# Optimization experiments

Measured on AMD Instinct MI355X. Metric: run time of the kernel, lower is better.

## Reference

```python
import jax, jax.numpy as jnp
import numpy as np
from jax import lax

CHANNEL = 64
HIDDEN = 128

def _conv(x, w, b):
    # x: [B, Cin, H, W], w: [Cout, Cin, 3, 3] -> [B, Cout, H, W], SAME padding
    y = lax.conv_general_dilated(x, w, window_strides=(1, 1), padding='SAME',
                                 dimension_numbers=('NCHW', 'OIHW', 'NCHW'))
    return y + b[None, :, None, None]

def setup_inputs() -> dict:
    key = jax.random.key(0)
    ks = jax.random.split(key, 5)
    T, B, C, H, W = 12, 2, CHANNEL, 128, 128
    x = jax.random.normal(ks[0], (T, B, C, H, W), dtype=jnp.float32)
    fan_g = (C + HIDDEN) * 9
    W_gates = jax.random.normal(ks[1], (4 * HIDDEN, C + HIDDEN, 3, 3), dtype=jnp.float32) / np.sqrt(fan_g)
    b_gates = jnp.zeros((4 * HIDDEN,), dtype=jnp.float32)
    W_out = jax.random.normal(ks[2], (C, HIDDEN, 3, 3), dtype=jnp.float32) / np.sqrt(HIDDEN * 9)
    b_out = jnp.zeros((C,), dtype=jnp.float32)
    return {'x': x, 'W_gates': W_gates, 'b_gates': b_gates, 'W_out': W_out, 'b_out': b_out}

def _convlstm_forward(x, W_gates, b_gates, W_out, b_out):
    T, B, C, H, W = x.shape
    h0 = jnp.zeros((B, HIDDEN, H, W), dtype=x.dtype)
    c0 = jnp.zeros((B, HIDDEN, H, W), dtype=x.dtype)

    def step(carry, xt):
        h, c = carry
        gates = _conv(jnp.concatenate([xt, h], axis=1), W_gates, b_gates)
        i_g, f_g, o_g, g_g = jnp.split(gates, 4, axis=1)
        c = jax.nn.sigmoid(f_g) * c + jax.nn.sigmoid(i_g) * jnp.tanh(g_g)
        h = jax.nn.sigmoid(o_g) * jnp.tanh(c)
        return (h, c), h

    _, hs = lax.scan(step, (h0, c0), x)          # hs: [T, B, HIDDEN, H, W]
    out = _conv(hs.reshape(T * B, HIDDEN, H, W), W_out, b_out)
    return out.reshape(T, B, C, H, W)

def reference(x, W_gates, b_gates, W_out, b_out):
    return _convlstm_forward(x, W_gates, b_gates, W_out, b_out)
```

## Files before the change

### kernel.cpp

```cpp
#include <hip/hip_runtime.h>

typedef _Float16 f16;
typedef __attribute__((ext_vector_type(8))) _Float16 f16x8;
typedef __attribute__((ext_vector_type(4))) _Float16 f16x4;
typedef __attribute__((ext_vector_type(4))) float f32x4;

#define SLICE_H 4326400


__device__ __forceinline__ void gld_lds16(void* lds, const void* g) {
  __builtin_amdgcn_global_load_lds(
      (const __attribute__((address_space(1))) void*)g,
      (__attribute__((address_space(3))) void*)lds, 16, 0, 0);
}

__device__ __forceinline__ float sigf(float v) { return 1.0f / (1.0f + __expf(-v)); }
__device__ __forceinline__ float tanh_fast(float v) { return 2.0f / (1.0f + __expf(-2.0f * v)) - 1.0f; }


__global__ __launch_bounds__(256) void kwt(const float* __restrict__ wsrc,
                                           f16* __restrict__ th, int R) {
  int idx = blockIdx.x * 256 + threadIdx.x;
  if (idx >= 9 * R) return;
  int tap = idx / R, r = idx - tap * R;
  th[idx] = (f16)wsrc[(size_t)r * 9 + tap];
}


__global__ __launch_bounds__(256) void kxform(const float* __restrict__ xt,
                                              f16* __restrict__ xp) {
  int pid = blockIdx.x * 256 + threadIdx.x;
  int b = pid >> 14, y = (pid >> 7) & 127, x = pid & 127;
  const float* src = xt + (size_t)b * 64 * 16384 + (size_t)y * 128 + x;
  size_t doff = ((size_t)((b * 130 + y + 1) * 130 + (x + 1))) * 64;
#pragma unroll
  for (int cc = 0; cc < 8; ++cc) {
    f16x8 vh;
#pragma unroll
    for (int j = 0; j < 8; ++j) vh[j] = (f16)src[(size_t)(cc * 8 + j) * 16384];
    *(f16x8*)(xp + doff + cc * 8) = vh;
  }
}


#define SMEM_G (25344 + 49152)

__global__ __launch_bounds__(512, 4) void kgates(
    const f16* __restrict__ xp, const f16* __restrict__ hp,
    const f16* __restrict__ wg, f16* __restrict__ gates) {
  extern __shared__ char smem[];
  f16* Ap = (f16*)smem;
  f16* Br = (f16*)(smem + 25344);
  const int tid = threadIdx.x;
  const int lane = tid & 63;
  const int w = tid >> 6;
  const int y = blockIdx.x;
  const int b = blockIdx.y;
  const int n0 = blockIdx.z * 256;
  const int wm = w >> 2, wn = w & 3;
  const int chunk = (lane & 3) ^ ((lane >> 3) & 3);

  f32x4 acc[4][4] = {};

  auto stageA = [&](int cig) {
    const f16* S; int CS, cigl;
    if (cig < 2) { S = xp; CS = 64;  cigl = cig; }
    else         { S = hp; CS = 128; cigl = cig - 2; }
    for (int i = w; i < 27; i += 8) {
      int dy = i / 9, sub = i - dy * 9;
      int xp0 = sub * 16;
      const f16* src = S +
          ((size_t)((b * 130 + y + dy) * 130 + xp0 + (lane >> 2))) * CS +
          cigl * 32 + chunk * 8;
      f16* dst = Ap + (dy * 132 + xp0) * 32;
      if (sub == 8) { if (lane < 16) gld_lds16(dst, src); }
      else gld_lds16(dst, src);
    }
  };
  auto stageB = [&](int j) {
    int cig = j / 9, tap = j - cig * 9;
    f16* dst = Br + (j % 3) * 8192;
    for (int i = w; i < 16; i += 8) {
      const f16* src = wg +
          ((size_t)(tap * 512 + n0 + i * 16 + (lane >> 2))) * 192 +
          cig * 32 + chunk * 8;
      gld_lds16(dst + i * 512, src);
    }
  };

  stageA(0);
  stageB(0);
  stageB(1);
  asm volatile("s_waitcnt vmcnt(2)" ::: "memory");
  __builtin_amdgcn_s_barrier();

  for (int j = 0; j < 54; ++j) {
    const int cig = j / 9, tap = j - cig * 9;
    const int dy = tap / 3, dx = tap - dy * 3;
    const int q = lane >> 4;
    const f16* Bc = Br + (j % 3) * 8192;
    f16x8 af[4], bfr[4];
#pragma unroll
    for (int mf = 0; mf < 4; ++mf) {
      int r = wm * 64 + mf * 16 + (lane & 15) + dx;
      af[mf] = *(const f16x8*)(Ap + (dy * 132 + r) * 32 + ((q ^ ((r >> 1) & 3)) << 3));
    }
#pragma unroll
    for (int nf = 0; nf < 4; ++nf) {
      int n = wn * 64 + nf * 16 + (lane & 15);
      bfr[nf] = *(const f16x8*)(Bc + n * 32 + ((q ^ ((n >> 1) & 3)) << 3));
    }
    if (j + 2 < 54) stageB(j + 2);
    __builtin_amdgcn_s_setprio(1);
#pragma unroll
    for (int mf = 0; mf < 4; ++mf)
#pragma unroll
      for (int nf = 0; nf < 4; ++nf)
        acc[mf][nf] = __builtin_amdgcn_mfma_f32_16x16x32_f16(af[mf], bfr[nf], acc[mf][nf], 0, 0, 0);
    __builtin_amdgcn_s_setprio(0);
    if (tap == 8) {
      __builtin_amdgcn_s_barrier();
      if (cig < 5) stageA(cig + 1);
      asm volatile("s_waitcnt vmcnt(0)" ::: "memory");
      __builtin_amdgcn_s_barrier();
    } else {
      if (j + 2 < 54) asm volatile("s_waitcnt vmcnt(2)" ::: "memory");
      else            asm volatile("s_waitcnt vmcnt(0)" ::: "memory");
      __builtin_amdgcn_s_barrier();
    }
  }

  size_t pixbase = ((size_t)(b * 128 + y)) * 128;
#pragma unroll
  for (int mf = 0; mf < 4; ++mf) {
#pragma unroll
    for (int nf = 0; nf < 4; ++nf) {
      int cout = n0 + wn * 64 + nf * 16 + (lane & 15);
#pragma unroll
      for (int r = 0; r < 4; ++r) {
        int x = wm * 64 + mf * 16 + (lane >> 4) * 4 + r;
        gates[(pixbase + x) * 512 + cout] = (f16)acc[mf][nf][r];
      }
    }
  }
}


__global__ __launch_bounds__(256) void kpoint(const f16* __restrict__ gates,
                                              const float* __restrict__ bg,
                                              float* __restrict__ cbuf,
                                              f16* __restrict__ hslot) {
  int gid = blockIdx.x * 256 + threadIdx.x;
  int pixel = gid >> 5, cq = gid & 31;
  int b = pixel >> 14, y = (pixel >> 7) & 127, x = pixel & 127;
  size_t gb = (size_t)pixel * 512 + cq * 4;
  const f16x4 ig = *(const f16x4*)(gates + gb);
  const f16x4 fg = *(const f16x4*)(gates + gb + 128);
  const f16x4 og = *(const f16x4*)(gates + gb + 256);
  const f16x4 gg = *(const f16x4*)(gates + gb + 384);
  const f32x4 bi  = *(const f32x4*)(bg + cq * 4);
  const f32x4 bff = *(const f32x4*)(bg + cq * 4 + 128);
  const f32x4 boo = *(const f32x4*)(bg + cq * 4 + 256);
  const f32x4 bgg = *(const f32x4*)(bg + cq * 4 + 384);
  f32x4 co = *(const f32x4*)(cbuf + (size_t)pixel * 128 + cq * 4);
  f32x4 cn;
  f16x4 hh;
#pragma unroll
  for (int j = 0; j < 4; ++j) {
    float iv = sigf((float)ig[j] + bi[j]);
    float fv = sigf((float)fg[j] + bff[j]);
    float ov = sigf((float)og[j] + boo[j]);
    float gv = tanh_fast((float)gg[j] + bgg[j]);
    float cv = fv * co[j] + iv * gv;
    float hv = ov * tanh_fast(cv);
    cn[j] = cv;
    hh[j] = (f16)hv;
  }
  *(f32x4*)(cbuf + (size_t)pixel * 128 + cq * 4) = cn;
  size_t hoff = ((size_t)((b * 130 + y + 1) * 130 + (x + 1))) * 128 + cq * 4;
  *(f16x4*)(hslot + hoff) = hh;
}


#define SMEM_O (25344 + 12288)

__global__ __launch_bounds__(256, 4) void koutconv(
    const f16* __restrict__ hr, int slot0, const f16* __restrict__ wo,
    const float* __restrict__ bo, float* __restrict__ outb) {
  extern __shared__ char smem[];
  f16* Ap = (f16*)smem;
  f16* Br = (f16*)(smem + 25344);
  const int tid = threadIdx.x, lane = tid & 63, w = tid >> 6;
  const int y = blockIdx.x;
  const int b = blockIdx.y;
  const int ts = blockIdx.z;
  const f16* hp = hr + (size_t)((slot0 + ts) % 5) * SLICE_H;
  float* outt = outb + (size_t)ts * 2 * 64 * 16384;
  const int chunk = (lane & 3) ^ ((lane >> 3) & 3);

  f32x4 acc[2][4] = {};

  auto stageA = [&](int cig) {
    for (int i = w; i < 27; i += 4) {
      int dy = i / 9, sub = i - dy * 9;
      int xp0 = sub * 16;
      const f16* src = hp +
          ((size_t)((b * 130 + y + dy) * 130 + xp0 + (lane >> 2))) * 128 +
          cig * 32 + chunk * 8;
      f16* dst = Ap + (dy * 132 + xp0) * 32;
      if (sub == 8) { if (lane < 16) gld_lds16(dst, src); }
      else gld_lds16(dst, src);
    }
  };
  auto stageB = [&](int j) {
    int cig = j / 9, tap = j - cig * 9;
    const f16* src = wo +
        ((size_t)(tap * 64 + w * 16 + (lane >> 2))) * 128 +
        cig * 32 + chunk * 8;
    gld_lds16(Br + (j % 3) * 2048 + w * 512, src);
  };

  stageA(0);
  stageB(0);
  stageB(1);
  asm volatile("s_waitcnt vmcnt(1)" ::: "memory");
  __builtin_amdgcn_s_barrier();

  for (int j = 0; j < 36; ++j) {
    const int cig = j / 9, tap = j - cig * 9;
    const int dy = tap / 3, dx = tap - dy * 3;
    const int q = lane >> 4;
    const f16* Bc = Br + (j % 3) * 2048;
    f16x8 af[2], bfr[4];
#pragma unroll
    for (int mf = 0; mf < 2; ++mf) {
      int r = w * 32 + mf * 16 + (lane & 15) + dx;
      af[mf] = *(const f16x8*)(Ap + (dy * 132 + r) * 32 + ((q ^ ((r >> 1) & 3)) << 3));
    }
#pragma unroll
    for (int nf = 0; nf < 4; ++nf) {
      int n = nf * 16 + (lane & 15);
      bfr[nf] = *(const f16x8*)(Bc + n * 32 + ((q ^ ((n >> 1) & 3)) << 3));
    }
    if (j + 2 < 36) stageB(j + 2);
    __builtin_amdgcn_s_setprio(1);
#pragma unroll
    for (int mf = 0; mf < 2; ++mf)
#pragma unroll
      for (int nf = 0; nf < 4; ++nf)
        acc[mf][nf] = __builtin_amdgcn_mfma_f32_16x16x32_f16(af[mf], bfr[nf], acc[mf][nf], 0, 0, 0);
    __builtin_amdgcn_s_setprio(0);
    if (tap == 8) {
      __builtin_amdgcn_s_barrier();
      if (cig < 3) stageA(cig + 1);
      asm volatile("s_waitcnt vmcnt(0)" ::: "memory");
      __builtin_amdgcn_s_barrier();
    } else {
      if (j + 2 < 36) asm volatile("s_waitcnt vmcnt(1)" ::: "memory");
      else            asm volatile("s_waitcnt vmcnt(0)" ::: "memory");
      __builtin_amdgcn_s_barrier();
    }
  }

#pragma unroll
  for (int nf = 0; nf < 4; ++nf) {
    int cout = nf * 16 + (lane & 15);
    float bias = bo[cout];
#pragma unroll
    for (int mf = 0; mf < 2; ++mf) {
      int xbase = w * 32 + mf * 16 + (lane >> 4) * 4;
      f32x4 v = acc[mf][nf];
      v[0] += bias; v[1] += bias; v[2] += bias; v[3] += bias;
      *(f32x4*)(outt + (((size_t)b * 64 + cout) * 128 + y) * 128 + xbase) = v;
    }
  }
}


extern "C" void kernel_launch(void* const* d_in, const int* in_sizes, int n_in,
                              void* d_out, int out_size, void* d_ws, size_t ws_size,
                              hipStream_t stream) {
  const float* x  = (const float*)d_in[0];
  const float* Wg = (const float*)d_in[1];
  const float* bg = (const float*)d_in[2];
  const float* Wo = (const float*)d_in[3];
  const float* bo = (const float*)d_in[4];
  float* out = (float*)d_out;

  char* base = (char*)d_ws;
  size_t off = 0;
  auto carve = [&](size_t bytes) {
    char* p = base + off;
    off += (bytes + 1023) & ~(size_t)1023;
    return p;
  };
  const size_t PADPOS = (size_t)2 * 130 * 130;
  const size_t xpad_b  = PADPOS * 64 * 2 + 1024;
  const size_t hring_b = (size_t)5 * SLICE_H * 2 + 1024;
  const size_t c_b = (size_t)2 * 128 * 128 * 128 * 4;
  const size_t g_b = (size_t)2 * 128 * 128 * 512 * 2;

  f16* xp    = (f16*)carve(xpad_b);
  f16* hr    = (f16*)carve(hring_b);
  float* cbuf = (float*)carve(c_b);
  f16* gates = (f16*)carve(g_b);
  f16* wg    = (f16*)carve((size_t)9 * 512 * 192 * 2);
  f16* wo    = (f16*)carve((size_t)9 * 64 * 128 * 2);

  hipMemsetAsync(xp, 0, xpad_b, stream);
  hipMemsetAsync(hr, 0, hring_b, stream);
  hipMemsetAsync(cbuf, 0, c_b, stream);

  kwt<<<(9 * 512 * 192 + 255) / 256, 256, 0, stream>>>(Wg, wg, 512 * 192);
  kwt<<<(9 * 64 * 128 + 255) / 256, 256, 0, stream>>>(Wo, wo, 64 * 128);

  for (int t = 0; t < 12; ++t) {
    const float* xt = x + (size_t)t * 2 * 64 * 16384;
    kxform<<<128, 256, 0, stream>>>(xt, xp);
    kgates<<<dim3(128, 2, 2), 512, SMEM_G, stream>>>(
        xp, hr + (size_t)(t % 5) * SLICE_H, wg, gates);
    kpoint<<<4096, 256, 0, stream>>>(gates, bg, cbuf,
        hr + (size_t)((t + 1) % 5) * SLICE_H);
    if ((t & 3) == 3) {
      koutconv<<<dim3(128, 2, 4), 256, SMEM_O, stream>>>(
          hr, (t - 2) % 5, wo, bo, out + (size_t)(t - 3) * 2 * 64 * 16384);
    }
  }
}
```

Before: 1.134 ms.

## Fuse LSTM pointwise update into gates conv epilogue via gate-interleaved weights

Reorders the gate weight rows so that each wave's output tile holds the i, f, o and g gates for the same 16 hidden channels. This lets the conv kernel apply the sigmoid/tanh cell update in registers and write c and h directly, removing the fp16 gates buffer round-trip and the separate pointwise launch per timestep. In exchange the block shrinks to 4 waves, each holding an 8x4 accumulator tile, which doubles accumulator registers per thread and halves waves per block. The loops are also restructured so the ring-buffer slot is tracked incrementally instead of computed with a modulo.

```diff
diff --git a/kernel.cpp b/kernel.cpp
--- a/kernel.cpp
+++ b/kernel.cpp
@@ -26,6 +26,18 @@
   th[idx] = (f16)wsrc[(size_t)r * 9 + tap];
 }
 
+__global__ __launch_bounds__(256) void kwtg(const float* __restrict__ wsrc,
+                                            f16* __restrict__ th) {
+  int idx = blockIdx.x * 256 + threadIdx.x;
+  const int R = 512 * 192;
+  if (idx >= 9 * R) return;
+  int tap = idx / R, rr = idx - tap * R;
+  int co = rr / 192, ci = rr - co * 192;
+  int gate = co >> 7, hch = co & 127;
+  int N = ((hch >> 6) << 8) + (((hch & 63) >> 4) << 6) + (gate << 4) + (hch & 15);
+  th[(size_t)tap * R + (size_t)N * 192 + ci] = (f16)wsrc[(size_t)rr * 9 + tap];
+}
+
 
 __global__ __launch_bounds__(256) void kxform(const float* __restrict__ xt,
                                               f16* __restrict__ xp) {
@@ -45,9 +57,10 @@
 
 #define SMEM_G (25344 + 49152)
 
-__global__ __launch_bounds__(512, 4) void kgates(
+__global__ __launch_bounds__(256, 2) void kgates(
     const f16* __restrict__ xp, const f16* __restrict__ hp,
-    const f16* __restrict__ wg, f16* __restrict__ gates) {
+    const f16* __restrict__ wg, const float* __restrict__ bg,
+    float* __restrict__ cbuf, f16* __restrict__ hslot) {
   extern __shared__ char smem[];
   f16* Ap = (f16*)smem;
   f16* Br = (f16*)(smem + 25344);
@@ -56,17 +69,17 @@
   const int w = tid >> 6;
   const int y = blockIdx.x;
   const int b = blockIdx.y;
-  const int n0 = blockIdx.z * 256;
-  const int wm = w >> 2, wn = w & 3;
+  const int z = blockIdx.z;
+  const int n0 = z * 256;
   const int chunk = (lane & 3) ^ ((lane >> 3) & 3);
 
-  f32x4 acc[4][4] = {};
+  f32x4 acc[8][4] = {};
 
   auto stageA = [&](int cig) {
     const f16* S; int CS, cigl;
     if (cig < 2) { S = xp; CS = 64;  cigl = cig; }
     else         { S = hp; CS = 128; cigl = cig - 2; }
-    for (int i = w; i < 27; i += 8) {
+    for (int i = w; i < 27; i += 4) {
       int dy = i / 9, sub = i - dy * 9;
       int xp0 = sub * 16;
       const f16* src = S +
@@ -77,10 +90,9 @@
       else gld_lds16(dst, src);
     }
   };
-  auto stageB = [&](int j) {
-    int cig = j / 9, tap = j - cig * 9;
-    f16* dst = Br + (j % 3) * 8192;
-    for (int i = w; i < 16; i += 8) {
+  auto stageB = [&](int cig, int tap, int slot) {
+    f16* dst = Br + slot * 8192;
+    for (int i = w; i < 16; i += 4) {
       const f16* src = wg +
           ((size_t)(tap * 512 + n0 + i * 16 + (lane >> 2))) * 192 +
           cig * 32 + chunk * 8;
@@ -89,96 +101,78 @@
   };
 
   stageA(0);
-  stageB(0);
-  stageB(1);
-  asm volatile("s_waitcnt vmcnt(2)" ::: "memory");
+  stageB(0, 0, 0);
+  stageB(0, 1, 1);
+  asm volatile("s_waitcnt vmcnt(4)" ::: "memory");
   __builtin_amdgcn_s_barrier();
 
-  for (int j = 0; j < 54; ++j) {
-    const int cig = j / 9, tap = j - cig * 9;
-    const int dy = tap / 3, dx = tap - dy * 3;
-    const int q = lane >> 4;
-    const f16* Bc = Br + (j % 3) * 8192;
-    f16x8 af[4], bfr[4];
-#pragma unroll
-    for (int mf = 0; mf < 4; ++mf) {
-      int r = wm * 64 + mf * 16 + (lane & 15) + dx;
-      af[mf] = *(const f16x8*)(Ap + (dy * 132 + r) * 32 + ((q ^ ((r >> 1) & 3)) << 3));
-    }
-#pragma unroll
-    for (int nf = 0; nf < 4; ++nf) {
-      int n = wn * 64 + nf * 16 + (lane & 15);
-      bfr[nf] = *(const f16x8*)(Bc + n * 32 + ((q ^ ((n >> 1) & 3)) << 3));
-    }
-    if (j + 2 < 54) stageB(j + 2);
-    __builtin_amdgcn_s_setprio(1);
-#pragma unroll
-    for (int mf = 0; mf < 4; ++mf)
-#pragma unroll
-      for (int nf = 0; nf < 4; ++nf)
-        acc[mf][nf] = __builtin_amdgcn_mfma_f32_16x16x32_f16(af[mf], bfr[nf], acc[mf][nf], 0, 0, 0);
-    __builtin_amdgcn_s_setprio(0);
-    if (tap == 8) {
-      __builtin_amdgcn_s_barrier();
-      if (cig < 5) stageA(cig + 1);
-      asm volatile("s_waitcnt vmcnt(0)" ::: "memory");
-      __builtin_amdgcn_s_barrier();
-    } else {
-      if (j + 2 < 54) asm volatile("s_waitcnt vmcnt(2)" ::: "memory");
-      else            asm volatile("s_waitcnt vmcnt(0)" ::: "memory");
-      __builtin_amdgcn_s_barrier();
-    }
-  }
-
-  size_t pixbase = ((size_t)(b * 128 + y)) * 128;
-#pragma unroll
-  for (int mf = 0; mf < 4; ++mf) {
-#pragma unroll
-    for (int nf = 0; nf < 4; ++nf) {
-      int cout = n0 + wn * 64 + nf * 16 + (lane & 15);
-#pragma unroll
-      for (int r = 0; r < 4; ++r) {
-        int x = wm * 64 + mf * 16 + (lane >> 4) * 4 + r;
-        gates[(pixbase + x) * 512 + cout] = (f16)acc[mf][nf][r];
-      }
-    }
-  }
-}
-
-
-__global__ __launch_bounds__(256) void kpoint(const f16* __restrict__ gates,
-                                              const float* __restrict__ bg,
-                                              float* __restrict__ cbuf,
-                                              f16* __restrict__ hslot) {
-  int gid = blockIdx.x * 256 + threadIdx.x;
-  int pixel = gid >> 5, cq = gid & 31;
-  int b = pixel >> 14, y = (pixel >> 7) & 127, x = pixel & 127;
-  size_t gb = (size_t)pixel * 512 + cq * 4;
-  const f16x4 ig = *(const f16x4*)(gates + gb);
-  const f16x4 fg = *(const f16x4*)(gates + gb + 128);
-  const f16x4 og = *(const f16x4*)(gates + gb + 256);
-  const f16x4 gg = *(const f16x4*)(gates + gb + 384);
-  const f32x4 bi  = *(const f32x4*)(bg + cq * 4);
-  const f32x4 bff = *(const f32x4*)(bg + cq * 4 + 128);
-  const f32x4 boo = *(const f32x4*)(bg + cq * 4 + 256);
-  const f32x4 bgg = *(const f32x4*)(bg + cq * 4 + 384);
-  f32x4 co = *(const f32x4*)(cbuf + (size_t)pixel * 128 + cq * 4);
-  f32x4 cn;
-  f16x4 hh;
-#pragma unroll
-  for (int j = 0; j < 4; ++j) {
-    float iv = sigf((float)ig[j] + bi[j]);
-    float fv = sigf((float)fg[j] + bff[j]);
-    float ov = sigf((float)og[j] + boo[j]);
-    float gv = tanh_fast((float)gg[j] + bgg[j]);
-    float cv = fv * co[j] + iv * gv;
-    float hv = ov * tanh_fast(cv);
-    cn[j] = cv;
-    hh[j] = (f16)hv;
-  }
-  *(f32x4*)(cbuf + (size_t)pixel * 128 + cq * 4) = cn;
-  size_t hoff = ((size_t)((b * 130 + y + 1) * 130 + (x + 1))) * 128 + cq * 4;
-  *(f16x4*)(hslot + hoff) = hh;
+  int sl = 0;
+  for (int cig = 0; cig < 6; ++cig) {
+    for (int tap = 0; tap < 9; ++tap) {
+      const int j = cig * 9 + tap;
+      const int dy = tap / 3, dx = tap - dy * 3;
+      const int q = lane >> 4;
+      const f16* Bc = Br + sl * 8192;
+      f16x8 af[8], bfr[4];
+#pragma unroll
+      for (int mf = 0; mf < 8; ++mf) {
+        int r = mf * 16 + (lane & 15) + dx;
+        af[mf] = *(const f16x8*)(Ap + (dy * 132 + r) * 32 + ((q ^ ((r >> 1) & 3)) << 3));
+      }
+#pragma unroll
+      for (int nf = 0; nf < 4; ++nf) {
+        int n = w * 64 + nf * 16 + (lane & 15);
+        bfr[nf] = *(const f16x8*)(Bc + n * 32 + ((q ^ ((n >> 1) & 3)) << 3));
+      }
+      if (j + 2 < 54) {
+        int j2 = j + 2;
+        stageB(j2 / 9, j2 % 9, (sl + 2 >= 3) ? sl - 1 : sl + 2);
+      }
+      __builtin_amdgcn_s_setprio(1);
+#pragma unroll
+      for (int mf = 0; mf < 8; ++mf)
+#pragma unroll
+        for (int nf = 0; nf < 4; ++nf)
+          acc[mf][nf] = __builtin_amdgcn_mfma_f32_16x16x32_f16(af[mf], bfr[nf], acc[mf][nf], 0, 0, 0);
+      __builtin_amdgcn_s_setprio(0);
+      if (tap == 8) {
+        __builtin_amdgcn_s_barrier();
+        if (cig < 5) stageA(cig + 1);
+        asm volatile("s_waitcnt vmcnt(0)" ::: "memory");
+        __builtin_amdgcn_s_barrier();
+      } else {
+        if (j + 2 < 54) asm volatile("s_waitcnt vmcnt(4)" ::: "memory");
+        else            asm volatile("s_waitcnt vmcnt(0)" ::: "memory");
+        __builtin_amdgcn_s_barrier();
+      }
+      sl = (sl + 1 >= 3) ? 0 : sl + 1;
+    }
+  }
+
+  const int lch = w * 16 + (lane & 15);
+  const int hch = z * 64 + lch;
+  const float bi  = bg[hch];
+  const float bf2 = bg[128 + hch];
+  const float bo2 = bg[256 + hch];
+  const float bg2 = bg[384 + hch];
+  const size_t pixbase = ((size_t)(b * 128 + y)) * 128;
+  const size_t hbase = ((size_t)((b * 130 + y + 1) * 130 + 1)) * 128 + hch;
+#pragma unroll
+  for (int mf = 0; mf < 8; ++mf) {
+#pragma unroll
+    for (int r = 0; r < 4; ++r) {
+      int px = mf * 16 + (lane >> 4) * 4 + r;
+      size_t cidx = (pixbase + px) * 128 + hch;
+      float co = cbuf[cidx];
+      float iv = sigf(acc[mf][0][r] + bi);
+      float fv = sigf(acc[mf][1][r] + bf2);
+      float ov = sigf(acc[mf][2][r] + bo2);
+      float gv = tanh_fast(acc[mf][3][r] + bg2);
+      float cv = fv * co + iv * gv;
+      cbuf[cidx] = cv;
+      hslot[hbase + (size_t)px * 128] = (f16)(ov * tanh_fast(cv));
+    }
+  }
 }
 
 
@@ -212,53 +206,57 @@
       else gld_lds16(dst, src);
     }
   };
-  auto stageB = [&](int j) {
+  auto stageB = [&](int j, int slot) {
     int cig = j / 9, tap = j - cig * 9;
     const f16* src = wo +
         ((size_t)(tap * 64 + w * 16 + (lane >> 2))) * 128 +
         cig * 32 + chunk * 8;
-    gld_lds16(Br + (j % 3) * 2048 + w * 512, src);
+    gld_lds16(Br + slot * 2048 + w * 512, src);
   };
 
   stageA(0);
-  stageB(0);
-  stageB(1);
+  stageB(0, 0);
+  stageB(1, 1);
   asm volatile("s_waitcnt vmcnt(1)" ::: "memory");
   __builtin_amdgcn_s_barrier();
 
-  for (int j = 0; j < 36; ++j) {
-    const int cig = j / 9, tap = j - cig * 9;
-    const int dy = tap / 3, dx = tap - dy * 3;
-    const int q = lane >> 4;
-    const f16* Bc = Br + (j % 3) * 2048;
-    f16x8 af[2], bfr[4];
-#pragma unroll
-    for (int mf = 0; mf < 2; ++mf) {
-      int r = w * 32 + mf * 16 + (lane & 15) + dx;
-      af[mf] = *(const f16x8*)(Ap + (dy * 132 + r) * 32 + ((q ^ ((r >> 1) & 3)) << 3));
-    }
-#pragma unroll
-    for (int nf = 0; nf < 4; ++nf) {
-      int n = nf * 16 + (lane & 15);
-      bfr[nf] = *(const f16x8*)(Bc + n * 32 + ((q ^ ((n >> 1) & 3)) << 3));
-    }
-    if (j + 2 < 36) stageB(j + 2);
-    __builtin_amdgcn_s_setprio(1);
-#pragma unroll
-    for (int mf = 0; mf < 2; ++mf)
-#pragma unroll
-      for (int nf = 0; nf < 4; ++nf)
-        acc[mf][nf] = __builtin_amdgcn_mfma_f32_16x16x32_f16(af[mf], bfr[nf], acc[mf][nf], 0, 0, 0);
-    __builtin_amdgcn_s_setprio(0);
-    if (tap == 8) {
-      __builtin_amdgcn_s_barrier();
-      if (cig < 3) stageA(cig + 1);
-      asm volatile("s_waitcnt vmcnt(0)" ::: "memory");
-      __builtin_amdgcn_s_barrier();
-    } else {
-      if (j + 2 < 36) asm volatile("s_waitcnt vmcnt(1)" ::: "memory");
-      else            asm volatile("s_waitcnt vmcnt(0)" ::: "memory");
-      __builtin_amdgcn_s_barrier();
+  int sl = 0;
+  for (int cig = 0; cig < 4; ++cig) {
+    for (int tap = 0; tap < 9; ++tap) {
+      const int j = cig * 9 + tap;
+      const int dy = tap / 3, dx = tap - dy * 3;
+      const int q = lane >> 4;
+      const f16* Bc = Br + sl * 2048;
+      f16x8 af[2], bfr[4];
+#pragma unroll
+      for (int mf = 0; mf < 2; ++mf) {
+        int r = w * 32 + mf * 16 + (lane & 15) + dx;
+        af[mf] = *(const f16x8*)(Ap + (dy * 132 + r) * 32 + ((q ^ ((r >> 1) & 3)) << 3));
+      }
+#pragma unroll
+      for (int nf = 0; nf < 4; ++nf) {
+        int n = nf * 16 + (lane & 15);
+        bfr[nf] = *(const f16x8*)(Bc + n * 32 + ((q ^ ((n >> 1) & 3)) << 3));
+      }
+      if (j + 2 < 36) stageB(j + 2, (sl + 2 >= 3) ? sl - 1 : sl + 2);
+      __builtin_amdgcn_s_setprio(1);
+#pragma unroll
+      for (int mf = 0; mf < 2; ++mf)
+#pragma unroll
+        for (int nf = 0; nf < 4; ++nf)
+          acc[mf][nf] = __builtin_amdgcn_mfma_f32_16x16x32_f16(af[mf], bfr[nf], acc[mf][nf], 0, 0, 0);
+      __builtin_amdgcn_s_setprio(0);
+      if (tap == 8) {
+        __builtin_amdgcn_s_barrier();
+        if (cig < 3) stageA(cig + 1);
+        asm volatile("s_waitcnt vmcnt(0)" ::: "memory");
+        __builtin_amdgcn_s_barrier();
+      } else {
+        if (j + 2 < 36) asm volatile("s_waitcnt vmcnt(1)" ::: "memory");
+        else            asm volatile("s_waitcnt vmcnt(0)" ::: "memory");
+        __builtin_amdgcn_s_barrier();
+      }
+      sl = (sl + 1 >= 3) ? 0 : sl + 1;
     }
   }
 
@@ -298,12 +296,10 @@
   const size_t xpad_b  = PADPOS * 64 * 2 + 1024;
   const size_t hring_b = (size_t)5 * SLICE_H * 2 + 1024;
   const size_t c_b = (size_t)2 * 128 * 128 * 128 * 4;
-  const size_t g_b = (size_t)2 * 128 * 128 * 512 * 2;
 
   f16* xp    = (f16*)carve(xpad_b);
   f16* hr    = (f16*)carve(hring_b);
   float* cbuf = (float*)carve(c_b);
-  f16* gates = (f16*)carve(g_b);
   f16* wg    = (f16*)carve((size_t)9 * 512 * 192 * 2);
   f16* wo    = (f16*)carve((size_t)9 * 64 * 128 * 2);
 
@@ -311,15 +307,14 @@
   hipMemsetAsync(hr, 0, hring_b, stream);
   hipMemsetAsync(cbuf, 0, c_b, stream);
 
-  kwt<<<(9 * 512 * 192 + 255) / 256, 256, 0, stream>>>(Wg, wg, 512 * 192);
+  kwtg<<<(9 * 512 * 192 + 255) / 256, 256, 0, stream>>>(Wg, wg);
   kwt<<<(9 * 64 * 128 + 255) / 256, 256, 0, stream>>>(Wo, wo, 64 * 128);
 
   for (int t = 0; t < 12; ++t) {
     const float* xt = x + (size_t)t * 2 * 64 * 16384;
     kxform<<<128, 256, 0, stream>>>(xt, xp);
-    kgates<<<dim3(128, 2, 2), 512, SMEM_G, stream>>>(
-        xp, hr + (size_t)(t % 5) * SLICE_H, wg, gates);
-    kpoint<<<4096, 256, 0, stream>>>(gates, bg, cbuf,
+    kgates<<<dim3(128, 2, 2), 256, SMEM_G, stream>>>(
+        xp, hr + (size_t)(t % 5) * SLICE_H, wg, bg, cbuf,
         hr + (size_t)((t + 1) % 5) * SLICE_H);
     if ((t & 3) == 3) {
       koutconv<<<dim3(128, 2, 4), 256, SMEM_O, stream>>>(
```

New measurement: 1.032 ms. 1.1x faster.
